# Performance work log

Hardware: AMD Instinct MI355X
Metric: run time of the kernel (lower is better)

## Reference

```python
import jax, jax.numpy as jnp
import numpy as np

B, S, D, H, L = 32, 512, 256, 8, 3
HD = D // H
FFN = D // 2
SCALE_BASE = 512.0
EPS = 1e-5


def _gammas():
    return (1.0 - jnp.exp(jnp.linspace(np.log(1.0 / 32.0), np.log(1.0 / 512.0), H))).astype(jnp.float32)


def _xpos(x, downscale):
    # x: [..., S, hd]; XPOS rotary embedding with exponential length scaling
    s, hd = x.shape[-2], x.shape[-1]
    half = hd // 2
    scale = (jnp.arange(0, hd, 2, dtype=jnp.float32) + 0.4 * hd) / (1.4 * hd)  # [half]
    power = jnp.arange(s, dtype=jnp.float32)[:, None] / SCALE_BASE
    sm = scale[None, :] ** power  # [S, half]
    if downscale:
        sm = 1.0 / sm
    inv_freq = 1.0 / (10000.0 ** (jnp.arange(half, dtype=jnp.float32) / half))
    ang = jnp.arange(s, dtype=jnp.float32)[:, None] * inv_freq[None, :]  # [S, half]
    sin = jnp.repeat(jnp.sin(ang) * sm, 2, axis=-1)  # duplicate_interleave -> [S, hd]
    cos = jnp.repeat(jnp.cos(ang) * sm, 2, axis=-1)
    x1, x2 = x[..., ::2], x[..., 1::2]
    rot = jnp.stack((-x2, x1), axis=-1).reshape(x.shape)  # rotate_every_two
    return x * cos + rot * sin


def _layer_norm(x, w, b):
    mu = x.mean(-1, keepdims=True)
    var = ((x - mu) ** 2).mean(-1, keepdims=True)
    return (x - mu) / jnp.sqrt(var + EPS) * w + b


def _msr(X, WQ, WK, WV, WG, WO, gn_w, gn_b):
    # Multi-scale retention, parallel form. X: [B,S,D]; WQ/WK/WV: [H,D,HD]
    b, s, _ = X.shape
    Q = _xpos(jnp.einsum('bsd,hde->bhse', X, WQ), False)
    K = _xpos(jnp.einsum('bsd,hde->bhse', X, WK), True)
    V = jnp.einsum('bsd,hde->bhse', X, WV)
    n = jnp.arange(s)
    delta = (n[:, None] - n[None, :]).astype(jnp.float32)
    mask = n[:, None] >= n[None, :]
    g = _gammas()
    Dm = jnp.where(mask[None], g[:, None, None] ** delta[None], 0.0)  # [H,S,S]
    scores = jnp.einsum('bhse,bhte->bhst', Q, K) * Dm[None]  # [B,H,S,S]
    Y = jnp.einsum('bhst,bhte->bhse', scores, V)  # [B,H,S,HD]
    Y = jnp.moveaxis(Y, 1, 2)  # [B,S,H,HD] (= concat heads)
    # GroupNorm(heads, v_dim): normalize per (token, head) group
    mu = Y.mean(-1, keepdims=True)
    var = ((Y - mu) ** 2).mean(-1, keepdims=True)
    Yn = ((Y - mu) / jnp.sqrt(var + EPS)).reshape(b, s, D) * gn_w + gn_b
    G = X @ WG
    return (G * jax.nn.sigmoid(G) * Yn) @ WO


def setup_inputs() -> dict:
    key = jax.random.key(0)
    ks = jax.random.split(key, 10)
    inp = {
        'v': jax.random.randint(ks[0], (B, S), 0, 65, dtype=jnp.int64),
        'emb': jax.random.normal(ks[1], (65, D), dtype=jnp.float32),
        'WQ': jax.random.normal(ks[2], (L, H, D, HD), dtype=jnp.float32) / D,
        'WK': jax.random.normal(ks[3], (L, H, D, HD), dtype=jnp.float32) / D,
        'WV': jax.random.normal(ks[4], (L, H, D, HD), dtype=jnp.float32) / D,
        'WG': jax.random.normal(ks[5], (L, D, D), dtype=jnp.float32) / D,
        'WO': jax.random.normal(ks[6], (L, D, D), dtype=jnp.float32) / D,
        'gn_w': jnp.ones((L, D), jnp.float32),
        'gn_b': jnp.zeros((L, D), jnp.float32),
        'ln1_w': jnp.ones((L, D), jnp.float32),
        'ln1_b': jnp.zeros((L, D), jnp.float32),
        'ln2_w': jnp.ones((L, D), jnp.float32),
        'ln2_b': jnp.zeros((L, D), jnp.float32),
        'w1': jax.random.normal(ks[7], (L, D, FFN), dtype=jnp.float32) * (1.0 / np.sqrt(D)),
        'b1': jnp.zeros((L, FFN), jnp.float32),
        'w2': jax.random.normal(ks[8], (L, FFN, D), dtype=jnp.float32) * (1.0 / np.sqrt(FFN)),
        'b2': jnp.zeros((L, D), jnp.float32),
    }
    return inp


def reference(v, emb, WQ, WK, WV, WG, WO, gn_w, gn_b, ln1_w, ln1_b, ln2_w, ln2_b, w1, b1, w2, b2):
    emb = emb.at[0].set(0.0)  # padding_idx=0
    X = jax.nn.relu(emb[v])  # [B,S,D]
    for i in range(L):
        Y = _msr(_layer_norm(X, ln1_w[i], ln1_b[i]), WQ[i], WK[i], WV[i], WG[i], WO[i], gn_w[i], gn_b[i]) + X
        h = jax.nn.gelu(_layer_norm(Y, ln2_w[i], ln2_b[i]) @ w1[i] + b1[i], approximate=False)
        X = h @ w2[i] + b2[i] + Y
    return X
```

## Files before the change

kernel.cpp:

```cpp
#include <hip/hip_runtime.h>
#include <hip/hip_bf16.h>
#include <math.h>

#define BB 32
#define SS 512
#define DD 256
#define HH 8
#define HDIM 32
#define FFNN 128
#define NROWS (BB*SS)
#define NELEM (NROWS*DD)

using bf16 = __hip_bfloat16;
typedef __attribute__((ext_vector_type(8))) short short8;
typedef __attribute__((ext_vector_type(4))) float floatx4;

static __device__ __forceinline__ float bf2f(bf16 x) { return __bfloat162float(x); }
static __device__ __forceinline__ bf16  f2bf(float x) { return __float2bfloat16(x); }
static __device__ __forceinline__ short f2bfs(float x) {
    bf16 b = __float2bfloat16(x);
    return __builtin_bit_cast(short, b);
}

static __device__ __forceinline__ void gld_lds16(const void* g, void* l) {
    __builtin_amdgcn_global_load_lds(
        (const __attribute__((address_space(1))) void*)g,
        (__attribute__((address_space(3))) void*)l, 16, 0, 0);
}

__global__ void init_flag(int* flag) { *flag = 0; }
__global__ __launch_bounds__(256) void detect_v(const int* __restrict__ v, int* __restrict__ flag) {
    int i = blockIdx.x * 256 + threadIdx.x;
    if (v[2 * i + 1] != 0) atomicOr(flag, 1);
}

#define NQKVG (3*1024*256)
#define NWO   (3*256*256)
#define NW1   (3*128*256)
#define NW2   (3*256*128)
#define NXPT  (512*16)
#define NSETUP (NQKVG+NWO+NW1+NW2+NXPT)
__global__ __launch_bounds__(256) void setup_pack(const float* __restrict__ WQ, const float* __restrict__ WK,
                                                  const float* __restrict__ WV, const float* __restrict__ WG,
                                                  const float* __restrict__ WO, const float* __restrict__ w1,
                                                  const float* __restrict__ w2,
                                                  bf16* __restrict__ dQ, bf16* __restrict__ dO,
                                                  bf16* __restrict__ d1, bf16* __restrict__ d2,
                                                  float4* __restrict__ xpt) {
    int idx = blockIdx.x * 256 + threadIdx.x;
    if (idx < NQKVG) {
        int k = idx & 255, n = (idx >> 8) & 1023, l = idx >> 18;
        int seg = n >> 8, n8 = n & 255;
        float val;
        if (seg < 3) {
            const float* W = (seg == 0) ? WQ : (seg == 1) ? WK : WV;
            int h = n8 >> 5, e = n8 & 31;
            val = W[(((size_t)l * 8 + h) * 256 + k) * 32 + e];
        } else {
            val = WG[(size_t)l * 65536 + k * 256 + n8];
        }
        dQ[((size_t)l * 1024 + n) * 256 + k] = f2bf(val);
    } else if (idx < NQKVG + NWO) {
        int i = idx - NQKVG;
        int k = i & 255, n = (i >> 8) & 255, l = i >> 16;
        dO[((size_t)l * 256 + n) * 256 + k] = f2bf(WO[(size_t)l * 65536 + k * 256 + n]);
    } else if (idx < NQKVG + NWO + NW1) {
        int i = idx - NQKVG - NWO;
        int k = i & 255, n = (i >> 8) & 127, l = i >> 15;
        d1[((size_t)l * 128 + n) * 256 + k] = f2bf(w1[(size_t)l * 32768 + k * 128 + n]);
    } else if (idx < NQKVG + NWO + NW1 + NW2) {
        int i = idx - NQKVG - NWO - NW1;
        int k = i & 127, n = (i >> 7) & 255, l = i >> 15;
        d2[((size_t)l * 256 + n) * 128 + k] = f2bf(w2[(size_t)l * 32768 + k * 256 + n]);
    } else {
        int i = idx - NQKVG - NWO - NW1 - NW2;
        int jf = i & 15, s = i >> 4;
        float base = (2.0f * jf + 12.8f) / 44.8f;
        float sm = powf(base, (float)s * (1.0f / 512.0f));
        float ang = (float)s * powf(10000.0f, -(float)jf / 16.0f);
        float sn, cs;
        sincosf(ang, &sn, &cs);
        xpt[i] = float4{cs * sm, sn * sm, cs / sm, sn / sm};
    }
}

__global__ __launch_bounds__(256) void embed_ln_kernel(const int* __restrict__ v,
                                                       const float* __restrict__ emb,
                                                       const int* __restrict__ flag,
                                                       const float* __restrict__ w,
                                                       const float* __restrict__ b,
                                                       float* __restrict__ X,
                                                       short* __restrict__ Xn) {
    int row = blockIdx.x;
    int d = threadIdx.x;
    int tok = (*flag) ? v[row] : v[2 * row];
    float x = 0.0f;
    if (tok != 0) {
        x = emb[tok * DD + d];
        x = x > 0.0f ? x : 0.0f;
    }
    X[(size_t)row * DD + d] = x;
    float s1 = x, s2 = x * x;
    #pragma unroll
    for (int off = 1; off < 64; off <<= 1) {
        s1 += __shfl_xor(s1, off);
        s2 += __shfl_xor(s2, off);
    }
    __shared__ float p1[4], p2[4], st[2];
    int wid = threadIdx.x >> 6;
    if ((threadIdx.x & 63) == 0) { p1[wid] = s1; p2[wid] = s2; }
    __syncthreads();
    if (threadIdx.x == 0) {
        float t1 = p1[0] + p1[1] + p1[2] + p1[3];
        float t2 = p2[0] + p2[1] + p2[2] + p2[3];
        float mu = t1 * (1.0f / DD);
        float var = t2 * (1.0f / DD) - mu * mu;
        st[0] = mu; st[1] = rsqrtf(var + 1e-5f);
    }
    __syncthreads();
    Xn[(size_t)row * DD + d] = f2bfs((x - st[0]) * st[1] * w[d] + b[d]);
}

__global__ __launch_bounds__(256) void qkvg_gemm(const short* __restrict__ A,
                                                 const short* __restrict__ Bp,
                                                 const float4* __restrict__ xpt,
                                                 bf16* __restrict__ C) {
    __shared__ __align__(16) short Als[16 * 512];
    __shared__ __align__(16) short Bls[16 * 512];
    const int tid = threadIdx.x;
    const int wave = tid >> 6, lane = tid & 63, lo = lane & 15, quad = lane >> 4;
    const int wm = wave >> 1, wn = wave & 1;
    const int row0 = blockIdx.x * 128, col0 = blockIdx.y * 128;

    floatx4 acc[4][4];
    #pragma unroll
    for (int i = 0; i < 4; ++i)
        #pragma unroll
        for (int j = 0; j < 4; ++j) acc[i][j] = floatx4{0.f, 0.f, 0.f, 0.f};

    for (int k0 = 0; k0 < 256; k0 += 64) {
        #pragma unroll
        for (int t = 0; t < 4; ++t) {
            int grp = (wm * 4 + t) * 2 + wn;
            const short* ga = A + (size_t)(row0 + (wm * 4 + t) * 16 + lo) * 256
                            + k0 + (wn * 4 + quad) * 8;
            gld_lds16(ga, &Als[grp * 512]);
        }
        #pragma unroll
        for (int t = 0; t < 4; ++t) {
            int grp = (wn * 4 + t) * 2 + wm;
            const short* gb = Bp + (size_t)(col0 + (wn * 4 + t) * 16 + lo) * 256
                            + k0 + (wm * 4 + quad) * 8;
            gld_lds16(gb, &Bls[grp * 512]);
        }
        __syncthreads();
        #pragma unroll
        for (int kkgrp = 0; kkgrp < 2; ++kkgrp) {
            short8 af[4], bfr[4];
            #pragma unroll
            for (int t = 0; t < 4; ++t)
                af[t] = *(const short8*)(&Als[((wm * 4 + t) * 2 + kkgrp) * 512 + lane * 8]);
            #pragma unroll
            for (int t = 0; t < 4; ++t)
                bfr[t] = *(const short8*)(&Bls[((wn * 4 + t) * 2 + kkgrp) * 512 + lane * 8]);
            #pragma unroll
            for (int ti = 0; ti < 4; ++ti)
                #pragma unroll
                for (int tj = 0; tj < 4; ++tj)
                    acc[ti][tj] = __builtin_amdgcn_mfma_f32_16x16x32_bf16(af[ti], bfr[tj], acc[ti][tj], 0, 0, 0);
        }
        __syncthreads();
    }

    #pragma unroll
    for (int ti = 0; ti < 4; ++ti) {
        #pragma unroll
        for (int tj = 0; tj < 4; ++tj) {
            int colb = col0 + (wn * 4 + tj) * 16 + lo;
            int seg = colb >> 8;
            #pragma unroll
            for (int r = 0; r < 4; ++r) {
                int row = row0 + (wm * 4 + ti) * 16 + quad * 4 + r;
                float v = acc[ti][tj][r];
                if (seg < 2) {
                    int s = row & (SS - 1);
                    int jf = (colb & 31) >> 1;
                    float4 t = xpt[s * 16 + jf];
                    float cs = (seg == 0) ? t.x : t.z;
                    float sn = (seg == 0) ? t.y : t.w;
                    float p = __shfl_xor(v, 1);
                    v = (lo & 1) ? (v * cs + p * sn) : (v * cs - p * sn);
                }
                C[(size_t)row * 1024 + colb] = f2bf(v);
            }
        }
    }
}

__global__ __launch_bounds__(256) void wo_gemm(const short* __restrict__ A,
                                               const short* __restrict__ Bp,
                                               float* __restrict__ X,
                                               const float* __restrict__ lnw,
                                               const float* __restrict__ lnb,
                                               short* __restrict__ Out) {
    __shared__ __align__(16) short Als[8 * 512];
    __shared__ __align__(16) short Bls[4][8 * 512];
    __shared__ float Ssum[64][4], Ssq[64][4];
    const int tid = threadIdx.x;
    const int wave = tid >> 6, lane = tid & 63, lo = lane & 15, quad = lane >> 4;
    const int row0 = blockIdx.x * 64;
    const int colw0 = wave * 64;

    floatx4 acc[4][4];
    #pragma unroll
    for (int i = 0; i < 4; ++i)
        #pragma unroll
        for (int j = 0; j < 4; ++j) acc[i][j] = floatx4{0.f, 0.f, 0.f, 0.f};

    const short* Ab = A + (size_t)(row0 + wave * 16 + lo) * 1024 + quad * 8;
    const short* Bb = Bp + (size_t)(colw0 + lo) * 256 + quad * 8;

    for (int k0 = 0; k0 < 256; k0 += 64) {
        gld_lds16(Ab + k0,      &Als[(wave * 2 + 0) * 512]);
        gld_lds16(Ab + k0 + 32, &Als[(wave * 2 + 1) * 512]);
        #pragma unroll
        for (int t = 0; t < 4; ++t)
            #pragma unroll
            for (int kk = 0; kk < 2; ++kk)
                gld_lds16(Bb + (size_t)(t * 16) * 256 + k0 + kk * 32,
                          &Bls[wave][(t * 2 + kk) * 512]);
        __syncthreads();
        #pragma unroll
        for (int kk = 0; kk < 2; ++kk) {
            short8 af[4], bfr[4];
            #pragma unroll
            for (int t = 0; t < 4; ++t)
                af[t] = *(const short8*)(&Als[(t * 2 + kk) * 512 + lane * 8]);
            #pragma unroll
            for (int t = 0; t < 4; ++t)
                bfr[t] = *(const short8*)(&Bls[wave][(t * 2 + kk) * 512 + lane * 8]);
            #pragma unroll
            for (int ti = 0; ti < 4; ++ti)
                #pragma unroll
                for (int tj = 0; tj < 4; ++tj)
                    acc[ti][tj] = __builtin_amdgcn_mfma_f32_16x16x32_bf16(af[ti], bfr[tj], acc[ti][tj], 0, 0, 0);
        }
        __syncthreads();
    }

    float vv[4][4][4];
    #pragma unroll
    for (int ti = 0; ti < 4; ++ti)
        #pragma unroll
        for (int tj = 0; tj < 4; ++tj) {
            int colb = colw0 + tj * 16 + lo;
            #pragma unroll
            for (int r = 0; r < 4; ++r) {
                int row = row0 + ti * 16 + quad * 4 + r;
                float v = acc[ti][tj][r] + X[(size_t)row * DD + colb];
                X[(size_t)row * DD + colb] = v;
                vv[ti][tj][r] = v;
            }
        }
    #pragma unroll
    for (int ti = 0; ti < 4; ++ti)
        #pragma unroll
        for (int r = 0; r < 4; ++r) {
            float s1 = 0.f, s2 = 0.f;
            #pragma unroll
            for (int tj = 0; tj < 4; ++tj) {
                float v = vv[ti][tj][r];
                s1 += v; s2 += v * v;
            }
            #pragma unroll
            for (int off = 1; off < 16; off <<= 1) {
                s1 += __shfl_xor(s1, off);
                s2 += __shfl_xor(s2, off);
            }
            if (lo == 0) {
                int rl = ti * 16 + quad * 4 + r;
                Ssum[rl][wave] = s1;
                Ssq[rl][wave] = s2;
            }
        }
    __syncthreads();
    #pragma unroll
    for (int ti = 0; ti < 4; ++ti)
        #pragma unroll
        for (int r = 0; r < 4; ++r) {
            int rl = ti * 16 + quad * 4 + r;
            float t1 = Ssum[rl][0] + Ssum[rl][1] + Ssum[rl][2] + Ssum[rl][3];
            float t2 = Ssq[rl][0] + Ssq[rl][1] + Ssq[rl][2] + Ssq[rl][3];
            float mu = t1 * (1.0f / DD);
            float var = t2 * (1.0f / DD) - mu * mu;
            float rs = rsqrtf(var + 1e-5f);
            int row = row0 + rl;
            #pragma unroll
            for (int tj = 0; tj < 4; ++tj) {
                int colb = colw0 + tj * 16 + lo;
                Out[(size_t)row * DD + colb] =
                    f2bfs((vv[ti][tj][r] - mu) * rs * lnw[colb] + lnb[colb]);
            }
        }
}

#define HSTR 136
template<int DOLN>
__global__ __launch_bounds__(256) void ffn_fused(const short* __restrict__ Xn,
                                                 const short* __restrict__ W1p,
                                                 const float* __restrict__ b1,
                                                 const short* __restrict__ W2p,
                                                 const float* __restrict__ b2,
                                                 float* __restrict__ X,
                                                 const float* __restrict__ lnw,
                                                 const float* __restrict__ lnb,
                                                 short* __restrict__ Out) {
    __shared__ __align__(16) short Als[8 * 512];
    __shared__ __align__(16) short Bls[4][8 * 512];
    __shared__ __align__(16) short Hls[64 * HSTR];
    __shared__ float Ssum[64][4], Ssq[64][4];
    const int tid = threadIdx.x;
    const int wave = tid >> 6, lane = tid & 63, lo = lane & 15, quad = lane >> 4;
    const int row0 = blockIdx.x * 64;

    floatx4 a1[4][2];
    #pragma unroll
    for (int i = 0; i < 4; ++i) { a1[i][0] = floatx4{0,0,0,0}; a1[i][1] = floatx4{0,0,0,0}; }
    const short* Ab = Xn + (size_t)(row0 + wave * 16 + lo) * 256 + quad * 8;
    const short* Bb1 = W1p + (size_t)(wave * 32 + lo) * 256 + quad * 8;
    for (int k0 = 0; k0 < 256; k0 += 64) {
        gld_lds16(Ab + k0,      &Als[(wave * 2 + 0) * 512]);
        gld_lds16(Ab + k0 + 32, &Als[(wave * 2 + 1) * 512]);
        #pragma unroll
        for (int t = 0; t < 2; ++t)
            #pragma unroll
            for (int kk = 0; kk < 2; ++kk)
                gld_lds16(Bb1 + (size_t)(t * 16) * 256 + k0 + kk * 32,
                          &Bls[wave][(t * 2 + kk) * 512]);
        __syncthreads();
        #pragma unroll
        for (int kk = 0; kk < 2; ++kk) {
            short8 af[4], bfr[2];
            #pragma unroll
            for (int t = 0; t < 4; ++t)
                af[t] = *(const short8*)(&Als[(t * 2 + kk) * 512 + lane * 8]);
            #pragma unroll
            for (int t = 0; t < 2; ++t)
                bfr[t] = *(const short8*)(&Bls[wave][(t * 2 + kk) * 512 + lane * 8]);
            #pragma unroll
            for (int ti = 0; ti < 4; ++ti)
                #pragma unroll
                for (int tj = 0; tj < 2; ++tj)
                    a1[ti][tj] = __builtin_amdgcn_mfma_f32_16x16x32_bf16(af[ti], bfr[tj], a1[ti][tj], 0, 0, 0);
        }
        __syncthreads();
    }
    #pragma unroll
    for (int ti = 0; ti < 4; ++ti)
        #pragma unroll
        for (int tj = 0; tj < 2; ++tj) {
            int colb = wave * 32 + tj * 16 + lo;
            float bs = b1[colb];
            #pragma unroll
            for (int r = 0; r < 4; ++r) {
                int rl = ti * 16 + quad * 4 + r;
                float v = a1[ti][tj][r] + bs;
                v = 0.5f * v * (1.0f + erff(v * 0.70710678118f));
                Hls[rl * HSTR + colb] = f2bfs(v);
            }
        }

    floatx4 a2[4][4];
    #pragma unroll
    for (int i = 0; i < 4; ++i)
        #pragma unroll
        for (int j = 0; j < 4; ++j) a2[i][j] = floatx4{0,0,0,0};
    const short* Bb2 = W2p + (size_t)(wave * 64 + lo) * 128 + quad * 8;
    for (int k0 = 0; k0 < 128; k0 += 64) {
        #pragma unroll
        for (int t = 0; t < 4; ++t)
            #pragma unroll
            for (int kk = 0; kk < 2; ++kk)
                gld_lds16(Bb2 + (size_t)(t * 16) * 128 + k0 + kk * 32,
                          &Bls[wave][(t * 2 + kk) * 512]);
        __syncthreads();
        #pragma unroll
        for (int kk = 0; kk < 2; ++kk) {
            short8 af[4], bfr[4];
            #pragma unroll
            for (int t = 0; t < 4; ++t)
                af[t] = *(const short8*)(&Hls[(t * 16 + lo) * HSTR + k0 + kk * 32 + quad * 8]);
            #pragma unroll
            for (int t = 0; t < 4; ++t)
                bfr[t] = *(const short8*)(&Bls[wave][(t * 2 + kk) * 512 + lane * 8]);
            #pragma unroll
            for (int ti = 0; ti < 4; ++ti)
                #pragma unroll
                for (int tj = 0; tj < 4; ++tj)
                    a2[ti][tj] = __builtin_amdgcn_mfma_f32_16x16x32_bf16(af[ti], bfr[tj], a2[ti][tj], 0, 0, 0);
        }
        __syncthreads();
    }

    float vv[4][4][4];
    #pragma unroll
    for (int ti = 0; ti < 4; ++ti)
        #pragma unroll
        for (int tj = 0; tj < 4; ++tj) {
            int colb = wave * 64 + tj * 16 + lo;
            float bs = b2[colb];
            #pragma unroll
            for (int r = 0; r < 4; ++r) {
                int row = row0 + ti * 16 + quad * 4 + r;
                float v = a2[ti][tj][r] + bs + X[(size_t)row * DD + colb];
                X[(size_t)row * DD + colb] = v;
                vv[ti][tj][r] = v;
            }
        }
    if (!DOLN) return;
    #pragma unroll
    for (int ti = 0; ti < 4; ++ti)
        #pragma unroll
        for (int r = 0; r < 4; ++r) {
            float s1 = 0.f, s2 = 0.f;
            #pragma unroll
            for (int tj = 0; tj < 4; ++tj) {
                float v = vv[ti][tj][r];
                s1 += v; s2 += v * v;
            }
            #pragma unroll
            for (int off = 1; off < 16; off <<= 1) {
                s1 += __shfl_xor(s1, off);
                s2 += __shfl_xor(s2, off);
            }
            if (lo == 0) {
                int rl = ti * 16 + quad * 4 + r;
                Ssum[rl][wave] = s1;
                Ssq[rl][wave] = s2;
            }
        }
    __syncthreads();
    #pragma unroll
    for (int ti = 0; ti < 4; ++ti)
        #pragma unroll
        for (int r = 0; r < 4; ++r) {
            int rl = ti * 16 + quad * 4 + r;
            float t1 = Ssum[rl][0] + Ssum[rl][1] + Ssum[rl][2] + Ssum[rl][3];
            float t2 = Ssq[rl][0] + Ssq[rl][1] + Ssq[rl][2] + Ssq[rl][3];
            float mu = t1 * (1.0f / DD);
            float var = t2 * (1.0f / DD) - mu * mu;
            float rs = rsqrtf(var + 1e-5f);
            int row = row0 + rl;
            #pragma unroll
            for (int tj = 0; tj < 4; ++tj) {
                int colb = wave * 64 + tj * 16 + lo;
                Out[(size_t)row * DD + colb] =
                    f2bfs((vv[ti][tj][r] - mu) * rs * lnw[colb] + lnb[colb]);
            }
        }
}

#define VSTRIDE 42
__global__ __launch_bounds__(256) void retention_mfma_kernel(bf16* __restrict__ QKVG,
                                                             const float* __restrict__ gnw,
                                                             const float* __restrict__ gnb) {
    __shared__ __align__(16) short Vl[4][32 * VSTRIDE];
    __shared__ __align__(16) short Pl[4][2 * 16 * 40];
    int wslot = threadIdx.x >> 6;
    int lane = threadIdx.x & 63;
    int qi = blockIdx.x >> 6;
    int bh = ((blockIdx.x & 63) << 2) | wslot;
    int b = bh >> 3, h = bh & 7;
    int q0 = qi * 32;
    int lo = lane & 15, quad = lane >> 4;

    const float la0 = -3.46573590280f, la1 = -6.23832462504f;
    float gamma = 1.0f - expf(la0 + (float)h * (la1 - la0) / 7.0f);
    float lg2 = log2f(gamma);
    float glo   = exp2f(-(float)lo * lg2);
    float g16i  = exp2f(-16.0f * lg2);
    float g16p  = exp2f(16.0f * lg2);
    float gi32  = exp2f(-32.0f * lg2);

    const size_t base = (size_t)b * SS * 1024;
    const short* QKVGs = (const short*)QKVG;

    short8 qfA = *(const short8*)(QKVGs + base + (size_t)(q0 + lo) * 1024 + h * HDIM + quad * 8);
    short8 qfB = *(const short8*)(QKVGs + base + (size_t)(q0 + 16 + lo) * 1024 + h * HDIM + quad * 8);

    float dA[4];
    #pragma unroll
    for (int r = 0; r < 4; ++r)
        dA[r] = exp2f((float)(q0 + quad * 4 + r) * lg2);

    floatx4 oA0 = {0,0,0,0}, oA1 = {0,0,0,0}, oB0 = {0,0,0,0}, oB1 = {0,0,0,0};
    short* Vw = Vl[wslot];
    short* PwA = Pl[wslot];
    short* PwB = Pl[wslot] + 16 * 40;
    int nch = qi + 1;

    for (int ch = 0; ch < nch; ++ch) {
        int t0 = ch * 32;
        const short* Kb = QKVGs + base + 256 + h * HDIM + quad * 8;
        short8 kf0 = *(const short8*)(Kb + (size_t)(t0 + lo) * 1024);
        short8 kf1 = *(const short8*)(Kb + (size_t)(t0 + 16 + lo) * 1024);
        {
            int r = lane >> 2, d = (lane & 3) * 8;
            const uint* Vg1 = (const uint*)(QKVGs + base + (size_t)(t0 + r) * 1024 + 512 + h * HDIM + d);
            const uint* Vg2 = (const uint*)(QKVGs + base + (size_t)(t0 + 16 + r) * 1024 + 512 + h * HDIM + d);
            uint* L1 = (uint*)(Vw + r * VSTRIDE + d);
            uint* L2 = (uint*)(Vw + (16 + r) * VSTRIDE + d);
            #pragma unroll
            for (int w = 0; w < 4; ++w) { L1[w] = Vg1[w]; L2[w] = Vg2[w]; }
        }
        floatx4 z = {0,0,0,0};
        floatx4 sA0 = __builtin_amdgcn_mfma_f32_16x16x32_bf16(qfA, kf0, z, 0, 0, 0);
        floatx4 sA1 = __builtin_amdgcn_mfma_f32_16x16x32_bf16(qfA, kf1, z, 0, 0, 0);
        floatx4 sB0 = __builtin_amdgcn_mfma_f32_16x16x32_bf16(qfB, kf0, z, 0, 0, 0);
        floatx4 sB1 = __builtin_amdgcn_mfma_f32_16x16x32_bf16(qfB, kf1, z, 0, 0, 0);
        #pragma unroll
        for (int r = 0; r < 4; ++r) {
            int qa = q0 + quad * 4 + r;
            int t = t0 + lo;
            float m = dA[r] * glo;
            float wA0 = (qa >= t)      ? m        : 0.0f;
            float wA1 = (qa >= t + 16) ? m * g16i : 0.0f;
            float wB0 = (qa + 16 >= t) ? m * g16p : 0.0f;
            PwA[(quad * 4 + r) * 40 + lo]      = f2bfs(sA0[r] * wA0);
            PwA[(quad * 4 + r) * 40 + 16 + lo] = f2bfs(sA1[r] * wA1);
            PwB[(quad * 4 + r) * 40 + lo]      = f2bfs(sB0[r] * wB0);
            PwB[(quad * 4 + r) * 40 + 16 + lo] = f2bfs(sB1[r] * wA0);
            dA[r] *= gi32;
        }
        __syncthreads();
        short8 pfA = *(const short8*)(PwA + lo * 40 + quad * 8);
        short8 pfB = *(const short8*)(PwB + lo * 40 + quad * 8);
        short8 vf0, vf1;
        #pragma unroll
        for (int j = 0; j < 8; ++j) {
            vf0[j] = Vw[(quad * 8 + j) * VSTRIDE + lo];
            vf1[j] = Vw[(quad * 8 + j) * VSTRIDE + 16 + lo];
        }
        oA0 = __builtin_amdgcn_mfma_f32_16x16x32_bf16(pfA, vf0, oA0, 0, 0, 0);
        oA1 = __builtin_amdgcn_mfma_f32_16x16x32_bf16(pfA, vf1, oA1, 0, 0, 0);
        oB0 = __builtin_amdgcn_mfma_f32_16x16x32_bf16(pfB, vf0, oB0, 0, 0, 0);
        oB1 = __builtin_amdgcn_mfma_f32_16x16x32_bf16(pfB, vf1, oB1, 0, 0, 0);
        __syncthreads();
    }

    float gw0 = gnw[h * HDIM + lo], gw1 = gnw[h * HDIM + 16 + lo];
    float gb0 = gnb[h * HDIM + lo], gb1 = gnb[h * HDIM + 16 + lo];
    bf16* QK = QKVG;
    #pragma unroll
    for (int sub = 0; sub < 2; ++sub) {
        floatx4 o0 = sub ? oB0 : oA0;
        floatx4 o1 = sub ? oB1 : oA1;
        int qbase = q0 + sub * 16;
        #pragma unroll
        for (int r = 0; r < 4; ++r) {
            float y0 = o0[r], y1 = o1[r];
            float s = y0 + y1, ss = y0 * y0 + y1 * y1;
            #pragma unroll
            for (int off = 1; off < 16; off <<= 1) {
                s  += __shfl_xor(s, off);
                ss += __shfl_xor(ss, off);
            }
            float mu = s * (1.0f / HDIM);
            float var = ss * (1.0f / HDIM) - mu * mu;
            float rstd = rsqrtf(var + 1e-5f);
            int q = qbase + quad * 4 + r;
            size_t rowb = base + (size_t)q * 1024;
            float g0 = bf2f(QK[rowb + 768 + h * HDIM + lo]);
            float g1 = bf2f(QK[rowb + 768 + h * HDIM + 16 + lo]);
            float t0v = g0 / (1.0f + expf(-g0)) * ((y0 - mu) * rstd * gw0 + gb0);
            float t1v = g1 / (1.0f + expf(-g1)) * ((y1 - mu) * rstd * gw1 + gb1);
            QK[rowb + h * HDIM + lo]      = f2bf(t0v);
            QK[rowb + h * HDIM + 16 + lo] = f2bf(t1v);
        }
    }
}

extern "C" void kernel_launch(void* const* d_in, const int* in_sizes, int n_in,
                              void* d_out, int out_size, void* d_ws, size_t ws_size,
                              hipStream_t stream) {
    const int*   v    = (const int*)d_in[0];
    const float* emb  = (const float*)d_in[1];
    const float* WQ   = (const float*)d_in[2];
    const float* WK   = (const float*)d_in[3];
    const float* WV   = (const float*)d_in[4];
    const float* WG   = (const float*)d_in[5];
    const float* WO   = (const float*)d_in[6];
    const float* gn_w = (const float*)d_in[7];
    const float* gn_b = (const float*)d_in[8];
    const float* ln1w = (const float*)d_in[9];
    const float* ln1b = (const float*)d_in[10];
    const float* ln2w = (const float*)d_in[11];
    const float* ln2b = (const float*)d_in[12];
    const float* w1   = (const float*)d_in[13];
    const float* b1   = (const float*)d_in[14];
    const float* w2   = (const float*)d_in[15];
    const float* b2   = (const float*)d_in[16];

    float* X = (float*)d_out;

    float* base  = (float*)d_ws;
    int*   flag  = (int*)base;
    short* Xn    = (short*)(base + 16);
    bf16*  QKVG  = (bf16*)(Xn + (size_t)NROWS * 256);
    bf16*  WqkvgP = QKVG + (size_t)NROWS * 1024;
    bf16*  WoP   = WqkvgP + 3 * 1024 * 256;
    bf16*  W1P   = WoP + 3 * 256 * 256;
    bf16*  W2P   = W1P + 3 * 128 * 256;
    float4* xpt  = (float4*)(W2P + 3 * 256 * 128);

    init_flag<<<1, 1, 0, stream>>>(flag);
    detect_v<<<32, 256, 0, stream>>>(v, flag);
    setup_pack<<<NSETUP / 256, 256, 0, stream>>>(WQ, WK, WV, WG, WO, w1, w2,
                                                 WqkvgP, WoP, W1P, W2P, xpt);
    embed_ln_kernel<<<NROWS, 256, 0, stream>>>(v, emb, flag, ln1w, ln1b, X, Xn);

    for (int i = 0; i < 3; ++i) {
        qkvg_gemm<<<dim3(128, 8), 256, 0, stream>>>(Xn,
                                                    (const short*)(WqkvgP + (size_t)i * 1024 * 256),
                                                    xpt, QKVG);
        retention_mfma_kernel<<<1024, 256, 0, stream>>>(QKVG, gn_w + i * DD, gn_b + i * DD);
        wo_gemm<<<NROWS / 64, 256, 0, stream>>>((const short*)QKVG,
                                                (const short*)(WoP + (size_t)i * 256 * 256),
                                                X, ln2w + i * DD, ln2b + i * DD, Xn);
        if (i < 2)
            ffn_fused<1><<<NROWS / 64, 256, 0, stream>>>(Xn,
                                                         (const short*)(W1P + (size_t)i * 128 * 256),
                                                         b1 + i * FFNN,
                                                         (const short*)(W2P + (size_t)i * 256 * 128),
                                                         b2 + i * DD, X,
                                                         ln1w + (i + 1) * DD, ln1b + (i + 1) * DD, Xn);
        else
            ffn_fused<0><<<NROWS / 64, 256, 0, stream>>>(Xn,
                                                         (const short*)(W1P + (size_t)i * 128 * 256),
                                                         b1 + i * FFNN,
                                                         (const short*)(W2P + (size_t)i * 256 * 128),
                                                         b2 + i * DD, X,
                                                         nullptr, nullptr, nullptr);
    }
}
```

Baseline: 410.6 us.

## Halve GEMM row tiles and restructure retention to keep scores in registers

The wo_gemm and ffn_fused kernels move from 64-row to 32-row blocks, doubling the grid to 512 blocks for better CU occupancy. The retention kernel now computes S^T (K as the A operand) so the masked, decayed scores can be packed straight into bf16 registers with v_cvt_pk_bf16_f32 and fed into 16x16x16 MFMAs. This drops the P shared-memory round trip and both per-chunk __syncthreads. Query-chunk order is reversed and interleaved so the heaviest causal chunks start first, and the decay mask is only applied on the diagonal chunk. Risks are more blocks re-reading the weight tiles and twice as many smaller MFMAs in the PV product.

```diff
diff --git a/kernel.cpp b/kernel.cpp
--- a/kernel.cpp
+++ b/kernel.cpp
@@ -13,13 +13,34 @@
 
 using bf16 = __hip_bfloat16;
 typedef __attribute__((ext_vector_type(8))) short short8;
+typedef __attribute__((ext_vector_type(4))) short short4v;
 typedef __attribute__((ext_vector_type(4))) float floatx4;
+typedef unsigned int uint_al __attribute__((may_alias));
 
 static __device__ __forceinline__ float bf2f(bf16 x) { return __bfloat162float(x); }
 static __device__ __forceinline__ bf16  f2bf(float x) { return __float2bfloat16(x); }
 static __device__ __forceinline__ short f2bfs(float x) {
     bf16 b = __float2bfloat16(x);
     return __builtin_bit_cast(short, b);
+}
+
+static __device__ __forceinline__ unsigned int cvtpk(float a, float b) {
+    unsigned int r;
+    asm("v_cvt_pk_bf16_f32 %0, %1, %2" : "=v"(r) : "v"(a), "v"(b));
+    return r;
+}
+static __device__ __forceinline__ short4v mk4(unsigned int a, unsigned int b) {
+    union { unsigned int u[2]; short4v s; } t;
+    t.u[0] = a; t.u[1] = b;
+    return t.s;
+}
+static __device__ __forceinline__ floatx4 mfma16(short4v a, short4v b, floatx4 c) {
+#if __has_builtin(__builtin_amdgcn_mfma_f32_16x16x16bf16_1k)
+    return __builtin_amdgcn_mfma_f32_16x16x16bf16_1k(a, b, c, 0, 0, 0);
+#else
+    asm("v_mfma_f32_16x16x16_bf16 %0, %1, %2, %0" : "+v"(c) : "v"(a), "v"(b));
+    return c;
+#endif
 }
 
 static __device__ __forceinline__ void gld_lds16(const void* g, void* l) {
@@ -203,26 +224,25 @@
                                                const float* __restrict__ lnw,
                                                const float* __restrict__ lnb,
                                                short* __restrict__ Out) {
-    __shared__ __align__(16) short Als[8 * 512];
+    __shared__ __align__(16) short Als[4 * 512];
     __shared__ __align__(16) short Bls[4][8 * 512];
-    __shared__ float Ssum[64][4], Ssq[64][4];
+    __shared__ float Ssum[32][4], Ssq[32][4];
     const int tid = threadIdx.x;
     const int wave = tid >> 6, lane = tid & 63, lo = lane & 15, quad = lane >> 4;
-    const int row0 = blockIdx.x * 64;
+    const int row0 = blockIdx.x * 32;
     const int colw0 = wave * 64;
 
-    floatx4 acc[4][4];
-    #pragma unroll
-    for (int i = 0; i < 4; ++i)
+    floatx4 acc[2][4];
+    #pragma unroll
+    for (int i = 0; i < 2; ++i)
         #pragma unroll
         for (int j = 0; j < 4; ++j) acc[i][j] = floatx4{0.f, 0.f, 0.f, 0.f};
 
-    const short* Ab = A + (size_t)(row0 + wave * 16 + lo) * 1024 + quad * 8;
+    const short* Ab = A + (size_t)(row0 + (wave >> 1) * 16 + lo) * 1024 + ((wave & 1) * 4 + quad) * 8;
     const short* Bb = Bp + (size_t)(colw0 + lo) * 256 + quad * 8;
 
     for (int k0 = 0; k0 < 256; k0 += 64) {
-        gld_lds16(Ab + k0,      &Als[(wave * 2 + 0) * 512]);
-        gld_lds16(Ab + k0 + 32, &Als[(wave * 2 + 1) * 512]);
+        gld_lds16(Ab + k0, &Als[wave * 512]);
         #pragma unroll
         for (int t = 0; t < 4; ++t)
             #pragma unroll
@@ -232,15 +252,15 @@
         __syncthreads();
         #pragma unroll
         for (int kk = 0; kk < 2; ++kk) {
-            short8 af[4], bfr[4];
-            #pragma unroll
-            for (int t = 0; t < 4; ++t)
+            short8 af[2], bfr[4];
+            #pragma unroll
+            for (int t = 0; t < 2; ++t)
                 af[t] = *(const short8*)(&Als[(t * 2 + kk) * 512 + lane * 8]);
             #pragma unroll
             for (int t = 0; t < 4; ++t)
                 bfr[t] = *(const short8*)(&Bls[wave][(t * 2 + kk) * 512 + lane * 8]);
             #pragma unroll
-            for (int ti = 0; ti < 4; ++ti)
+            for (int ti = 0; ti < 2; ++ti)
                 #pragma unroll
                 for (int tj = 0; tj < 4; ++tj)
                     acc[ti][tj] = __builtin_amdgcn_mfma_f32_16x16x32_bf16(af[ti], bfr[tj], acc[ti][tj], 0, 0, 0);
@@ -248,9 +268,9 @@
         __syncthreads();
     }
 
-    float vv[4][4][4];
-    #pragma unroll
-    for (int ti = 0; ti < 4; ++ti)
+    float vv[2][4][4];
+    #pragma unroll
+    for (int ti = 0; ti < 2; ++ti)
         #pragma unroll
         for (int tj = 0; tj < 4; ++tj) {
             int colb = colw0 + tj * 16 + lo;
@@ -263,7 +283,7 @@
             }
         }
     #pragma unroll
-    for (int ti = 0; ti < 4; ++ti)
+    for (int ti = 0; ti < 2; ++ti)
         #pragma unroll
         for (int r = 0; r < 4; ++r) {
             float s1 = 0.f, s2 = 0.f;
@@ -285,7 +305,7 @@
         }
     __syncthreads();
     #pragma unroll
-    for (int ti = 0; ti < 4; ++ti)
+    for (int ti = 0; ti < 2; ++ti)
         #pragma unroll
         for (int r = 0; r < 4; ++r) {
             int rl = ti * 16 + quad * 4 + r;
@@ -315,22 +335,21 @@
                                                  const float* __restrict__ lnw,
                                                  const float* __restrict__ lnb,
                                                  short* __restrict__ Out) {
-    __shared__ __align__(16) short Als[8 * 512];
+    __shared__ __align__(16) short Als[4 * 512];
     __shared__ __align__(16) short Bls[4][8 * 512];
-    __shared__ __align__(16) short Hls[64 * HSTR];
-    __shared__ float Ssum[64][4], Ssq[64][4];
+    __shared__ __align__(16) short Hls[32 * HSTR];
+    __shared__ float Ssum[32][4], Ssq[32][4];
     const int tid = threadIdx.x;
     const int wave = tid >> 6, lane = tid & 63, lo = lane & 15, quad = lane >> 4;
-    const int row0 = blockIdx.x * 64;
-
-    floatx4 a1[4][2];
-    #pragma unroll
-    for (int i = 0; i < 4; ++i) { a1[i][0] = floatx4{0,0,0,0}; a1[i][1] = floatx4{0,0,0,0}; }
-    const short* Ab = Xn + (size_t)(row0 + wave * 16 + lo) * 256 + quad * 8;
+    const int row0 = blockIdx.x * 32;
+
+    floatx4 a1[2][2];
+    #pragma unroll
+    for (int i = 0; i < 2; ++i) { a1[i][0] = floatx4{0,0,0,0}; a1[i][1] = floatx4{0,0,0,0}; }
+    const short* Ab = Xn + (size_t)(row0 + (wave >> 1) * 16 + lo) * 256 + ((wave & 1) * 4 + quad) * 8;
     const short* Bb1 = W1p + (size_t)(wave * 32 + lo) * 256 + quad * 8;
     for (int k0 = 0; k0 < 256; k0 += 64) {
-        gld_lds16(Ab + k0,      &Als[(wave * 2 + 0) * 512]);
-        gld_lds16(Ab + k0 + 32, &Als[(wave * 2 + 1) * 512]);
+        gld_lds16(Ab + k0, &Als[wave * 512]);
         #pragma unroll
         for (int t = 0; t < 2; ++t)
             #pragma unroll
@@ -340,15 +359,15 @@
         __syncthreads();
         #pragma unroll
         for (int kk = 0; kk < 2; ++kk) {
-            short8 af[4], bfr[2];
-            #pragma unroll
-            for (int t = 0; t < 4; ++t)
+            short8 af[2], bfr[2];
+            #pragma unroll
+            for (int t = 0; t < 2; ++t)
                 af[t] = *(const short8*)(&Als[(t * 2 + kk) * 512 + lane * 8]);
             #pragma unroll
             for (int t = 0; t < 2; ++t)
                 bfr[t] = *(const short8*)(&Bls[wave][(t * 2 + kk) * 512 + lane * 8]);
             #pragma unroll
-            for (int ti = 0; ti < 4; ++ti)
+            for (int ti = 0; ti < 2; ++ti)
                 #pragma unroll
                 for (int tj = 0; tj < 2; ++tj)
                     a1[ti][tj] = __builtin_amdgcn_mfma_f32_16x16x32_bf16(af[ti], bfr[tj], a1[ti][tj], 0, 0, 0);
@@ -356,7 +375,7 @@
         __syncthreads();
     }
     #pragma unroll
-    for (int ti = 0; ti < 4; ++ti)
+    for (int ti = 0; ti < 2; ++ti)
         #pragma unroll
         for (int tj = 0; tj < 2; ++tj) {
             int colb = wave * 32 + tj * 16 + lo;
@@ -370,9 +389,9 @@
             }
         }
 
-    floatx4 a2[4][4];
-    #pragma unroll
-    for (int i = 0; i < 4; ++i)
+    floatx4 a2[2][4];
+    #pragma unroll
+    for (int i = 0; i < 2; ++i)
         #pragma unroll
         for (int j = 0; j < 4; ++j) a2[i][j] = floatx4{0,0,0,0};
     const short* Bb2 = W2p + (size_t)(wave * 64 + lo) * 128 + quad * 8;
@@ -386,15 +405,15 @@
         __syncthreads();
         #pragma unroll
         for (int kk = 0; kk < 2; ++kk) {
-            short8 af[4], bfr[4];
-            #pragma unroll
-            for (int t = 0; t < 4; ++t)
+            short8 af[2], bfr[4];
+            #pragma unroll
+            for (int t = 0; t < 2; ++t)
                 af[t] = *(const short8*)(&Hls[(t * 16 + lo) * HSTR + k0 + kk * 32 + quad * 8]);
             #pragma unroll
             for (int t = 0; t < 4; ++t)
                 bfr[t] = *(const short8*)(&Bls[wave][(t * 2 + kk) * 512 + lane * 8]);
             #pragma unroll
-            for (int ti = 0; ti < 4; ++ti)
+            for (int ti = 0; ti < 2; ++ti)
                 #pragma unroll
                 for (int tj = 0; tj < 4; ++tj)
                     a2[ti][tj] = __builtin_amdgcn_mfma_f32_16x16x32_bf16(af[ti], bfr[tj], a2[ti][tj], 0, 0, 0);
@@ -402,9 +421,9 @@
         __syncthreads();
     }
 
-    float vv[4][4][4];
-    #pragma unroll
-    for (int ti = 0; ti < 4; ++ti)
+    float vv[2][4][4];
+    #pragma unroll
+    for (int ti = 0; ti < 2; ++ti)
         #pragma unroll
         for (int tj = 0; tj < 4; ++tj) {
             int colb = wave * 64 + tj * 16 + lo;
@@ -419,7 +438,7 @@
         }
     if (!DOLN) return;
     #pragma unroll
-    for (int ti = 0; ti < 4; ++ti)
+    for (int ti = 0; ti < 2; ++ti)
         #pragma unroll
         for (int r = 0; r < 4; ++r) {
             float s1 = 0.f, s2 = 0.f;
@@ -441,7 +460,7 @@
         }
     __syncthreads();
     #pragma unroll
-    for (int ti = 0; ti < 4; ++ti)
+    for (int ti = 0; ti < 2; ++ti)
         #pragma unroll
         for (int r = 0; r < 4; ++r) {
             int rl = ti * 16 + quad * 4 + r;
@@ -460,27 +479,34 @@
         }
 }
 
-#define VSTRIDE 42
+#define VSTR 44
 __global__ __launch_bounds__(256) void retention_mfma_kernel(bf16* __restrict__ QKVG,
                                                              const float* __restrict__ gnw,
                                                              const float* __restrict__ gnb) {
-    __shared__ __align__(16) short Vl[4][32 * VSTRIDE];
-    __shared__ __align__(16) short Pl[4][2 * 16 * 40];
-    int wslot = threadIdx.x >> 6;
-    int lane = threadIdx.x & 63;
-    int qi = blockIdx.x >> 6;
-    int bh = ((blockIdx.x & 63) << 2) | wslot;
-    int b = bh >> 3, h = bh & 7;
-    int q0 = qi * 32;
-    int lo = lane & 15, quad = lane >> 4;
+    __shared__ __align__(16) short Vt[4][32 * VSTR];
+    const int wslot = threadIdx.x >> 6;
+    const int lane = threadIdx.x & 63;
+    const int gblk = blockIdx.x >> 6;
+    const int qi = 15 - ((gblk & ~3) + (((gblk & 3) + (gblk >> 2)) & 3));
+    const int bh = ((blockIdx.x & 63) << 2) | wslot;
+    const int b = bh >> 3, h = bh & 7;
+    const int q0 = qi * 32;
+    const int lo = lane & 15, quad = lane >> 4;
 
     const float la0 = -3.46573590280f, la1 = -6.23832462504f;
     float gamma = 1.0f - expf(la0 + (float)h * (la1 - la0) / 7.0f);
     float lg2 = log2f(gamma);
-    float glo   = exp2f(-(float)lo * lg2);
-    float g16i  = exp2f(-16.0f * lg2);
-    float g16p  = exp2f(16.0f * lg2);
-    float gi32  = exp2f(-32.0f * lg2);
+    float g16i = exp2f(-16.0f * lg2);
+    float g16p = exp2f(16.0f * lg2);
+    float gi32 = exp2f(-32.0f * lg2);
+    float wq[4], wq16[4], wqB[4];
+    #pragma unroll
+    for (int r = 0; r < 4; ++r) {
+        wq[r]   = exp2f((float)(lo - 4 * quad - r) * lg2);
+        wq16[r] = wq[r] * g16i;
+        wqB[r]  = wq[r] * g16p;
+    }
+    float c = exp2f((float)q0 * lg2);
 
     const size_t base = (size_t)b * SS * 1024;
     const short* QKVGs = (const short*)QKVG;
@@ -488,64 +514,74 @@
     short8 qfA = *(const short8*)(QKVGs + base + (size_t)(q0 + lo) * 1024 + h * HDIM + quad * 8);
     short8 qfB = *(const short8*)(QKVGs + base + (size_t)(q0 + 16 + lo) * 1024 + h * HDIM + quad * 8);
 
-    float dA[4];
-    #pragma unroll
-    for (int r = 0; r < 4; ++r)
-        dA[r] = exp2f((float)(q0 + quad * 4 + r) * lg2);
-
     floatx4 oA0 = {0,0,0,0}, oA1 = {0,0,0,0}, oB0 = {0,0,0,0}, oB1 = {0,0,0,0};
-    short* Vw = Vl[wslot];
-    short* PwA = Pl[wslot];
-    short* PwB = Pl[wslot] + 16 * 40;
-    int nch = qi + 1;
+    short* Vw = Vt[wslot];
+    const int nch = qi + 1;
 
     for (int ch = 0; ch < nch; ++ch) {
-        int t0 = ch * 32;
+        const int t0 = ch * 32;
         const short* Kb = QKVGs + base + 256 + h * HDIM + quad * 8;
         short8 kf0 = *(const short8*)(Kb + (size_t)(t0 + lo) * 1024);
         short8 kf1 = *(const short8*)(Kb + (size_t)(t0 + 16 + lo) * 1024);
         {
-            int r = lane >> 2, d = (lane & 3) * 8;
-            const uint* Vg1 = (const uint*)(QKVGs + base + (size_t)(t0 + r) * 1024 + 512 + h * HDIM + d);
-            const uint* Vg2 = (const uint*)(QKVGs + base + (size_t)(t0 + 16 + r) * 1024 + 512 + h * HDIM + d);
-            uint* L1 = (uint*)(Vw + r * VSTRIDE + d);
-            uint* L2 = (uint*)(Vw + (16 + r) * VSTRIDE + d);
-            #pragma unroll
-            for (int w = 0; w < 4; ++w) { L1[w] = Vg1[w]; L2[w] = Vg2[w]; }
-        }
-        floatx4 z = {0,0,0,0};
-        floatx4 sA0 = __builtin_amdgcn_mfma_f32_16x16x32_bf16(qfA, kf0, z, 0, 0, 0);
-        floatx4 sA1 = __builtin_amdgcn_mfma_f32_16x16x32_bf16(qfA, kf1, z, 0, 0, 0);
-        floatx4 sB0 = __builtin_amdgcn_mfma_f32_16x16x32_bf16(qfB, kf0, z, 0, 0, 0);
-        floatx4 sB1 = __builtin_amdgcn_mfma_f32_16x16x32_bf16(qfB, kf1, z, 0, 0, 0);
+            const int r = lane >> 2, dcol = (lane & 3) * 8;
+            const short* Vg = QKVGs + base + 512 + h * HDIM + dcol;
+            uint4 u1 = *(const uint4*)(Vg + (size_t)(t0 + r) * 1024);
+            uint4 u2 = *(const uint4*)(Vg + (size_t)(t0 + 16 + r) * 1024);
+            uint_al* W1 = (uint_al*)(Vw + r * VSTR + dcol);
+            uint_al* W2 = (uint_al*)(Vw + (16 + r) * VSTR + dcol);
+            W1[0] = u1.x; W1[1] = u1.y; W1[2] = u1.z; W1[3] = u1.w;
+            W2[0] = u2.x; W2[1] = u2.y; W2[2] = u2.z; W2[3] = u2.w;
+        }
+        const floatx4 z = {0,0,0,0};
+        floatx4 sA0 = __builtin_amdgcn_mfma_f32_16x16x32_bf16(kf0, qfA, z, 0, 0, 0);
+        floatx4 sA1 = __builtin_amdgcn_mfma_f32_16x16x32_bf16(kf1, qfA, z, 0, 0, 0);
+        floatx4 sB0 = __builtin_amdgcn_mfma_f32_16x16x32_bf16(kf0, qfB, z, 0, 0, 0);
+        floatx4 sB1 = __builtin_amdgcn_mfma_f32_16x16x32_bf16(kf1, qfB, z, 0, 0, 0);
+
+        float m0[4], m1[4], mB[4];
         #pragma unroll
         for (int r = 0; r < 4; ++r) {
-            int qa = q0 + quad * 4 + r;
-            int t = t0 + lo;
-            float m = dA[r] * glo;
-            float wA0 = (qa >= t)      ? m        : 0.0f;
-            float wA1 = (qa >= t + 16) ? m * g16i : 0.0f;
-            float wB0 = (qa + 16 >= t) ? m * g16p : 0.0f;
-            PwA[(quad * 4 + r) * 40 + lo]      = f2bfs(sA0[r] * wA0);
-            PwA[(quad * 4 + r) * 40 + 16 + lo] = f2bfs(sA1[r] * wA1);
-            PwB[(quad * 4 + r) * 40 + lo]      = f2bfs(sB0[r] * wB0);
-            PwB[(quad * 4 + r) * 40 + 16 + lo] = f2bfs(sB1[r] * wA0);
-            dA[r] *= gi32;
-        }
-        __syncthreads();
-        short8 pfA = *(const short8*)(PwA + lo * 40 + quad * 8);
-        short8 pfB = *(const short8*)(PwB + lo * 40 + quad * 8);
-        short8 vf0, vf1;
-        #pragma unroll
-        for (int j = 0; j < 8; ++j) {
-            vf0[j] = Vw[(quad * 8 + j) * VSTRIDE + lo];
-            vf1[j] = Vw[(quad * 8 + j) * VSTRIDE + 16 + lo];
-        }
-        oA0 = __builtin_amdgcn_mfma_f32_16x16x32_bf16(pfA, vf0, oA0, 0, 0, 0);
-        oA1 = __builtin_amdgcn_mfma_f32_16x16x32_bf16(pfA, vf1, oA1, 0, 0, 0);
-        oB0 = __builtin_amdgcn_mfma_f32_16x16x32_bf16(pfB, vf0, oB0, 0, 0, 0);
-        oB1 = __builtin_amdgcn_mfma_f32_16x16x32_bf16(pfB, vf1, oB1, 0, 0, 0);
-        __syncthreads();
+            m0[r] = c * wq[r];
+            m1[r] = c * wq16[r];
+            mB[r] = c * wqB[r];
+        }
+        if (ch == qi) {
+            #pragma unroll
+            for (int r = 0; r < 4; ++r) {
+                if (lo < 4 * quad + r) m0[r] = 0.0f;
+                m1[r] = 0.0f;
+            }
+        }
+        c *= gi32;
+
+        unsigned int pa0 = cvtpk(sA0[0] * m0[0], sA0[1] * m0[1]);
+        unsigned int pa1 = cvtpk(sA0[2] * m0[2], sA0[3] * m0[3]);
+        unsigned int pa2 = cvtpk(sA1[0] * m1[0], sA1[1] * m1[1]);
+        unsigned int pa3 = cvtpk(sA1[2] * m1[2], sA1[3] * m1[3]);
+        unsigned int pb0 = cvtpk(sB0[0] * mB[0], sB0[1] * mB[1]);
+        unsigned int pb1 = cvtpk(sB0[2] * mB[2], sB0[3] * mB[3]);
+        unsigned int pb2 = cvtpk(sB1[0] * m0[0], sB1[1] * m0[1]);
+        unsigned int pb3 = cvtpk(sB1[2] * m0[2], sB1[3] * m0[3]);
+        short4v pA0 = mk4(pa0, pa1), pA1 = mk4(pa2, pa3);
+        short4v pB0 = mk4(pb0, pb1), pB1 = mk4(pb2, pb3);
+
+        short4v v00, v01, v10, v11;
+        #pragma unroll
+        for (int j = 0; j < 4; ++j) {
+            v00[j] = Vw[(4 * quad + j) * VSTR + lo];
+            v01[j] = Vw[(16 + 4 * quad + j) * VSTR + lo];
+            v10[j] = Vw[(4 * quad + j) * VSTR + 16 + lo];
+            v11[j] = Vw[(16 + 4 * quad + j) * VSTR + 16 + lo];
+        }
+        oA0 = mfma16(pA0, v00, oA0);
+        oA0 = mfma16(pA1, v01, oA0);
+        oA1 = mfma16(pA0, v10, oA1);
+        oA1 = mfma16(pA1, v11, oA1);
+        oB0 = mfma16(pB0, v00, oB0);
+        oB0 = mfma16(pB1, v01, oB0);
+        oB1 = mfma16(pB0, v10, oB1);
+        oB1 = mfma16(pB1, v11, oB1);
     }
 
     float gw0 = gnw[h * HDIM + lo], gw1 = gnw[h * HDIM + 16 + lo];
@@ -624,18 +660,18 @@
                                                     (const short*)(WqkvgP + (size_t)i * 1024 * 256),
                                                     xpt, QKVG);
         retention_mfma_kernel<<<1024, 256, 0, stream>>>(QKVG, gn_w + i * DD, gn_b + i * DD);
-        wo_gemm<<<NROWS / 64, 256, 0, stream>>>((const short*)QKVG,
+        wo_gemm<<<NROWS / 32, 256, 0, stream>>>((const short*)QKVG,
                                                 (const short*)(WoP + (size_t)i * 256 * 256),
                                                 X, ln2w + i * DD, ln2b + i * DD, Xn);
         if (i < 2)
-            ffn_fused<1><<<NROWS / 64, 256, 0, stream>>>(Xn,
+            ffn_fused<1><<<NROWS / 32, 256, 0, stream>>>(Xn,
                                                          (const short*)(W1P + (size_t)i * 128 * 256),
                                                          b1 + i * FFNN,
                                                          (const short*)(W2P + (size_t)i * 256 * 128),
                                                          b2 + i * DD, X,
                                                          ln1w + (i + 1) * DD, ln1b + (i + 1) * DD, Xn);
         else
-            ffn_fused<0><<<NROWS / 64, 256, 0, stream>>>(Xn,
+            ffn_fused<0><<<NROWS / 32, 256, 0, stream>>>(Xn,
                                                          (const short*)(W1P + (size_t)i * 128 * 256),
                                                          b1 + i * FFNN,
                                                          (const short*)(W2P + (size_t)i * 256 * 128),
```

New measurement: 396.4 us. 1.04x faster.
